# Performance work log

Measured on AMD Instinct MI355X. Metric: run time of the kernel, lower is better.

## Reference

```python
import jax, jax.numpy as jnp
import numpy as np

N_NODES = 100000
N_EDGES = 1600000


def gcn_conv(x, edge_index, W, b, num_nodes):
    # PyG GCNConv: add self-loops, symmetric deg^-1/2 normalization, linear, scatter-add, bias
    h = x @ W  # [N, out]
    loop = jnp.arange(num_nodes)
    row = jnp.concatenate([edge_index[0], loop])
    col = jnp.concatenate([edge_index[1], loop])
    deg = jax.ops.segment_sum(jnp.ones_like(col, dtype=h.dtype), col, num_segments=num_nodes)
    dinv = jnp.where(deg > 0, deg ** -0.5, 0.0)
    norm = dinv[row] * dinv[col]  # [E+N]
    msg = h[row] * norm[:, None]  # gather + scale
    out = jax.ops.segment_sum(msg, col, num_segments=num_nodes)
    return out + b


def setup_inputs() -> dict:
    key = jax.random.key(0)
    ks = jax.random.split(key, 12)
    x = jax.random.normal(ks[0], (N_NODES, 2), dtype=jnp.float32)
    edge_index = jax.random.randint(ks[1], (2, N_EDGES), 0, N_NODES, dtype=jnp.int64)
    edge_attr = jax.random.uniform(ks[2], (N_EDGES, 1), dtype=jnp.float32)
    W1 = jax.random.normal(ks[3], (2, 64), dtype=jnp.float32) * 0.5
    b1 = jnp.zeros((64,), dtype=jnp.float32)
    W2 = jax.random.normal(ks[4], (64, 32), dtype=jnp.float32) * (64 ** -0.5)
    b2 = jnp.zeros((32,), dtype=jnp.float32)
    mW1 = jax.random.normal(ks[5], (65, 16), dtype=jnp.float32) * (65 ** -0.5)
    mb1 = jnp.zeros((16,), dtype=jnp.float32)
    mW2 = jax.random.normal(ks[6], (16, 1), dtype=jnp.float32) * (16 ** -0.5)
    mb2 = jnp.zeros((1,), dtype=jnp.float32)
    return {"x": x, "edge_index": edge_index, "edge_attr": edge_attr,
            "num_nodes": N_NODES,
            "W1": W1, "b1": b1, "W2": W2, "b2": b2,
            "mW1": mW1, "mb1": mb1, "mW2": mW2, "mb2": mb2}


def reference(x, edge_index, edge_attr, num_nodes, W1, b1, W2, b2, mW1, mb1, mW2, mb2):
    h = jax.nn.relu(gcn_conv(x, edge_index, W1, b1, num_nodes))
    h = jax.nn.relu(gcn_conv(h, edge_index, W2, b2, num_nodes))
    row, col = edge_index[0], edge_index[1]
    ef = jnp.concatenate([h[row], h[col], edge_attr], axis=1)  # [E, 65]
    hid = jax.nn.relu(ef @ mW1 + mb1)
    return jax.nn.sigmoid(hid @ mW2 + mb2)  # [E, 1]
```

## Files before the change

kernel.cpp:

```cpp
#include <hip/hip_runtime.h>
#include <hip/hip_fp16.h>
#include <math.h>


__global__ void k_count(const int* __restrict__ col, int* __restrict__ deg, int E) {
    int stride = gridDim.x * blockDim.x;
    for (int e = blockIdx.x * blockDim.x + threadIdx.x; e < E; e += stride)
        atomicAdd(deg + col[e], 1);
}

__global__ void k_scan1(const int* __restrict__ deg, int* __restrict__ start,
                        int* __restrict__ bsum, int N) {
    __shared__ int sd[256];
    int t = threadIdx.x;
    int n = blockIdx.x * 256 + t;
    int d = (n < N) ? deg[n] : 0;
    sd[t] = d;
    __syncthreads();
    for (int off = 1; off < 256; off <<= 1) {
        int tv = (t >= off) ? sd[t - off] : 0;
        __syncthreads();
        sd[t] += tv;
        __syncthreads();
    }
    if (n < N) start[n] = sd[t] - d;
    if (t == 255) bsum[blockIdx.x] = sd[255];
}

__global__ void k_scan2(int* __restrict__ bsum, int nb) {
    __shared__ int sd[512];
    int t = threadIdx.x;
    int d = (t < nb) ? bsum[t] : 0;
    sd[t] = d;
    __syncthreads();
    for (int off = 1; off < 512; off <<= 1) {
        int tv = (t >= off) ? sd[t - off] : 0;
        __syncthreads();
        sd[t] += tv;
        __syncthreads();
    }
    if (t < nb) bsum[t] = sd[t] - d;
}

__global__ void k_scan3(int* __restrict__ start, const int* __restrict__ bsum,
                        int* __restrict__ cursor, const int* __restrict__ deg,
                        const float* __restrict__ x, float* __restrict__ dinv,
                        float* __restrict__ xs, int N) {
    int n = blockIdx.x * 256 + threadIdx.x;
    if (n >= N) return;
    int s = start[n] + bsum[blockIdx.x];
    start[n] = s;
    cursor[n] = s;
    float di = rsqrtf((float)deg[n] + 1.0f);
    dinv[n] = di;
    xs[2 * n] = x[2 * n] * di;
    xs[2 * n + 1] = x[2 * n + 1] * di;
}

__global__ void k_fill(const int* __restrict__ row, const int* __restrict__ col,
                       int* __restrict__ cursor, int* __restrict__ srcidx,
                       int E, int wshift, int nph) {
    int g      = blockIdx.x & 7;
    int tid0   = (blockIdx.x >> 3) * blockDim.x + threadIdx.x;
    int stride = (gridDim.x >> 3) * blockDim.x;
    for (int ph = g; ph < nph; ph += 8) {
        for (int e = tid0; e < E; e += stride) {
            int c = col[e];
            if ((c >> wshift) == ph) {
                int p = atomicAdd(cursor + c, 1);
                srcidx[p] = row[e];
            }
        }
    }
}

__global__ void k_l1l2(const int* __restrict__ start, const int* __restrict__ deg,
                       const int* __restrict__ srcidx,
                       const float* __restrict__ xs, const float* __restrict__ dinv,
                       const float* __restrict__ W1, const float* __restrict__ b1,
                       const float* __restrict__ W2,
                       __half* __restrict__ hs2h, int N) {
    __shared__ float sW1[128], sb1[64], sW2[2048];
    for (int i = threadIdx.x; i < 128;  i += blockDim.x) sW1[i] = W1[i];
    for (int i = threadIdx.x; i < 64;   i += blockDim.x) sb1[i] = b1[i];
    for (int i = threadIdx.x; i < 2048; i += blockDim.x) sW2[i] = W2[i];
    __syncthreads();
    int n = blockIdx.x * 256 + threadIdx.x;
    if (n >= N) return;
    int s = start[n], cnt = deg[n];
    float a0 = xs[2 * n], a1 = xs[2 * n + 1];
    for (int k = 0; k < cnt; ++k) {
        int r = srcidx[s + k];
        a0 += xs[2 * r];
        a1 += xs[2 * r + 1];
    }
    float di = dinv[n];
    a0 *= di; a1 *= di;
    float acc[32];
#pragma unroll
    for (int j = 0; j < 32; ++j) acc[j] = 0.0f;
    for (int k = 0; k < 64; ++k) {
        float h = fmaxf(fmaf(a0, sW1[k], fmaf(a1, sW1[64 + k], sb1[k])), 0.0f);
#pragma unroll
        for (int j = 0; j < 32; ++j) acc[j] = fmaf(h, sW2[k * 32 + j], acc[j]);
    }
    __half2 hb[16];
#pragma unroll
    for (int j = 0; j < 16; ++j)
        hb[j] = __floats2half2_rn(acc[2 * j] * di, acc[2 * j + 1] * di);
    float4* op = (float4*)(hs2h + (size_t)n * 32);
    const float4* ip = (const float4*)hb;
#pragma unroll
    for (int q = 0; q < 4; ++q) op[q] = ip[q];
}

__global__ void k_agg2uv(const int* __restrict__ start, const int* __restrict__ deg,
                         const int* __restrict__ srcidx,
                         const __half* __restrict__ hs2h, const float* __restrict__ dinv,
                         const float* __restrict__ b2, const float* __restrict__ mW1,
                         __half* __restrict__ u16, __half* __restrict__ v16, int N) {
    __shared__ float sA[512], sB[512], sb2[32];
    for (int i = threadIdx.x; i < 512; i += 256) { sA[i] = mW1[i]; sB[i] = mW1[512 + i]; }
    if (threadIdx.x < 32) sb2[threadIdx.x] = b2[threadIdx.x];
    __syncthreads();
    int L  = threadIdx.x & 63;
    int w  = threadIdx.x >> 6;
    int ch = L & 31;
    int h  = L >> 5;
    int n  = blockIdx.x * 4 + w;
    if (n >= N) return;

    int s = start[n], cnt = deg[n];
    float acc0 = (h == 0) ? __half2float(hs2h[(size_t)n * 32 + ch]) : 0.0f;
    float acc1 = 0.0f;
    int k = 0;
    for (; k + 3 < cnt; k += 4) {
        int ra = srcidx[s + k + h];
        int rb = srcidx[s + k + 2 + h];
        acc0 += __half2float(hs2h[(size_t)ra * 32 + ch]);
        acc1 += __half2float(hs2h[(size_t)rb * 32 + ch]);
    }
    for (; k + 1 < cnt; k += 2) {
        int r = srcidx[s + k + h];
        acc0 += __half2float(hs2h[(size_t)r * 32 + ch]);
    }
    if (k < cnt && h == 0) {
        int r = srcidx[s + k];
        acc0 += __half2float(hs2h[(size_t)r * 32 + ch]);
    }
    float acc = acc0 + acc1;
    acc += __shfl_xor(acc, 32);
    float h2 = fmaxf(fmaf(acc, dinv[n], sb2[ch]), 0.0f);

    int jh = L >> 5;
    int os = (L >> 4) & 1;
    int i  = L & 15;
    const float* M = os ? sB : sA;
    float part = 0.0f;
#pragma unroll
    for (int t = 0; t < 16; ++t) {
        int j = jh * 16 + t;
        float hj = __shfl(h2, j);
        part = fmaf(hj, M[j * 16 + i], part);
    }
    part += __shfl_xor(part, 32);
    if (L < 32) {
        __half val = __float2half_rn(part);
        if (os == 0) u16[(size_t)n * 16 + i] = val;
        else         v16[(size_t)n * 16 + i] = val;
    }
}

__device__ inline void unpack8(const float4 f, float* o) {
    const __half2* h2 = (const __half2*)&f;
#pragma unroll
    for (int i = 0; i < 4; ++i) {
        float2 t = __half22float2(h2[i]);
        o[2 * i] = t.x; o[2 * i + 1] = t.y;
    }
}

__global__ void k_edge(const int* __restrict__ row, const int* __restrict__ col,
                       const float* __restrict__ ea,
                       const __half* __restrict__ u16, const __half* __restrict__ v16,
                       const float* __restrict__ mW1, const float* __restrict__ mb1,
                       const float* __restrict__ mW2, const float* __restrict__ mb2,
                       float* __restrict__ out, int E) {
    __shared__ float sC[16], sb1[16], sW2v[16], sb2s;
    if (threadIdx.x < 16) {
        sC[threadIdx.x]   = mW1[64 * 16 + threadIdx.x];
        sb1[threadIdx.x]  = mb1[threadIdx.x];
        sW2v[threadIdx.x] = mW2[threadIdx.x];
    }
    if (threadIdx.x == 0) sb2s = mb2[0];
    __syncthreads();
    int tid    = blockIdx.x * blockDim.x + threadIdx.x;
    int stride = gridDim.x * blockDim.x;
    for (int e0 = tid * 2; e0 < E; e0 += stride * 2) {
        int e1 = e0 + 1;
        bool two = (e1 < E);
        int2 r2 = *(const int2*)(row + e0);
        int2 c2 = *(const int2*)(col + e0);
        float2 a2 = *(const float2*)(ea + e0);
        const float4* up0 = (const float4*)(u16 + (size_t)r2.x * 16);
        const float4* vp0 = (const float4*)(v16 + (size_t)c2.x * 16);
        const float4* up1 = (const float4*)(u16 + (size_t)r2.y * 16);
        const float4* vp1 = (const float4*)(v16 + (size_t)c2.y * 16);
        float4 ua0 = up0[0], ub0 = up0[1];
        float4 va0 = vp0[0], vb0 = vp0[1];
        float4 ua1 = up1[0], ub1 = up1[1];
        float4 va1 = vp1[0], vb1 = vp1[1];
        float uf0[16], vf0[16], uf1[16], vf1[16];
        unpack8(ua0, uf0); unpack8(ub0, uf0 + 8);
        unpack8(va0, vf0); unpack8(vb0, vf0 + 8);
        unpack8(ua1, uf1); unpack8(ub1, uf1 + 8);
        unpack8(va1, vf1); unpack8(vb1, vf1 + 8);
        float s0 = sb2s, s1 = sb2s;
#pragma unroll
        for (int i = 0; i < 16; ++i) {
            float t0 = fmaf(a2.x, sC[i], sb1[i]);
            float t1 = fmaf(a2.y, sC[i], sb1[i]);
            float h0 = fmaxf(uf0[i] + vf0[i] + t0, 0.0f);
            float h1 = fmaxf(uf1[i] + vf1[i] + t1, 0.0f);
            s0 = fmaf(h0, sW2v[i], s0);
            s1 = fmaf(h1, sW2v[i], s1);
        }
        float o0 = 1.0f / (1.0f + expf(-s0));
        float o1 = 1.0f / (1.0f + expf(-s1));
        if (two) {
            *(float2*)(out + e0) = make_float2(o0, o1);
        } else {
            out[e0] = o0;
        }
    }
}

extern "C" void kernel_launch(void* const* d_in, const int* in_sizes, int n_in,
                              void* d_out, int out_size, void* d_ws, size_t ws_size,
                              hipStream_t stream) {
    const float* x   = (const float*)d_in[0];
    const int*   ei  = (const int*)d_in[1];
    const float* ea  = (const float*)d_in[2];
    const float* W1  = (const float*)d_in[4];
    const float* b1  = (const float*)d_in[5];
    const float* W2  = (const float*)d_in[6];
    const float* b2  = (const float*)d_in[7];
    const float* mW1 = (const float*)d_in[8];
    const float* mb1 = (const float*)d_in[9];
    const float* mW2 = (const float*)d_in[10];
    const float* mb2 = (const float*)d_in[11];
    float* out = (float*)d_out;

    int N = in_sizes[0] / 2;
    int E = in_sizes[2];
    const int* row = ei;
    const int* col = ei + E;

    int clog = 0; while ((1u << clog) < (unsigned)N) ++clog;
    int wshift = clog > 3 ? clog - 3 : 0;
    int nph = ((N - 1) >> wshift) + 1;

    int* deg    = (int*)d_ws;
    int* start  = deg + N;
    int* cursor = start + N;
    int* bsum   = cursor + N;
    int* srcidx = bsum + 1024;
    float* dinv = (float*)(srcidx + E);
    float* xs   = dinv + (size_t)N;
    __half* hs2h = (__half*)(xs + (size_t)2 * N);
    __half* u16  = hs2h + (size_t)32 * N;
    __half* v16  = u16 + (size_t)16 * N;

    int nb_n = (N + 255) / 256;

    hipMemsetAsync(deg, 0, (size_t)N * sizeof(int), stream);
    k_count<<<2048, 256, 0, stream>>>(col, deg, E);
    k_scan1<<<nb_n, 256, 0, stream>>>(deg, start, bsum, N);
    k_scan2<<<1, 512, 0, stream>>>(bsum, nb_n);
    k_scan3<<<nb_n, 256, 0, stream>>>(start, bsum, cursor, deg, x, dinv, xs, N);
    k_fill <<<2048, 256, 0, stream>>>(row, col, cursor, srcidx, E, wshift, nph);
    k_l1l2 <<<nb_n, 256, 0, stream>>>(start, deg, srcidx, xs, dinv, W1, b1, W2, hs2h, N);
    k_agg2uv<<<(N + 3) / 4, 256, 0, stream>>>(start, deg, srcidx, hs2h, dinv, b2, mW1, u16, v16, N);
    k_edge <<<2048, 256, 0, stream>>>(row, col, ea, u16, v16, mW1, mb1, mW2, mb2, out, E);
}
```

Baseline: 365.8 us.

## Split edge MLP into two half-width passes for cache-resident node tables

The per-node u/v projection tables are split into two 8-channel halves, and the edge kernel runs twice. The first pass writes partial logits to a per-edge scratch buffer, and the second adds the rest and applies the sigmoid. Each pass's gather table is half as large, so the randomly gathered node data fits better in cache. The cost is re-reading the edge indices and edge attributes, plus an extra write and read of per-edge partial sums. The aggregation loop is also unrolled to four independent accumulators to expose more memory-level parallelism.

```diff
diff --git a/kernel.cpp b/kernel.cpp
--- a/kernel.cpp
+++ b/kernel.cpp
@@ -118,7 +118,8 @@
                          const int* __restrict__ srcidx,
                          const __half* __restrict__ hs2h, const float* __restrict__ dinv,
                          const float* __restrict__ b2, const float* __restrict__ mW1,
-                         __half* __restrict__ u16, __half* __restrict__ v16, int N) {
+                         __half* __restrict__ uA, __half* __restrict__ uB,
+                         __half* __restrict__ vA, __half* __restrict__ vB, int N) {
     __shared__ float sA[512], sB[512], sb2[32];
     for (int i = threadIdx.x; i < 512; i += 256) { sA[i] = mW1[i]; sB[i] = mW1[512 + i]; }
     if (threadIdx.x < 32) sb2[threadIdx.x] = b2[threadIdx.x];
@@ -132,13 +133,17 @@
 
     int s = start[n], cnt = deg[n];
     float acc0 = (h == 0) ? __half2float(hs2h[(size_t)n * 32 + ch]) : 0.0f;
-    float acc1 = 0.0f;
+    float acc1 = 0.0f, acc2 = 0.0f, acc3 = 0.0f;
     int k = 0;
-    for (; k + 3 < cnt; k += 4) {
+    for (; k + 7 < cnt; k += 8) {
         int ra = srcidx[s + k + h];
         int rb = srcidx[s + k + 2 + h];
+        int rc = srcidx[s + k + 4 + h];
+        int rd = srcidx[s + k + 6 + h];
         acc0 += __half2float(hs2h[(size_t)ra * 32 + ch]);
         acc1 += __half2float(hs2h[(size_t)rb * 32 + ch]);
+        acc2 += __half2float(hs2h[(size_t)rc * 32 + ch]);
+        acc3 += __half2float(hs2h[(size_t)rd * 32 + ch]);
     }
     for (; k + 1 < cnt; k += 2) {
         int r = srcidx[s + k + h];
@@ -148,7 +153,7 @@
         int r = srcidx[s + k];
         acc0 += __half2float(hs2h[(size_t)r * 32 + ch]);
     }
-    float acc = acc0 + acc1;
+    float acc = (acc0 + acc1) + (acc2 + acc3);
     acc += __shfl_xor(acc, 32);
     float h2 = fmaxf(fmaf(acc, dinv[n], sb2[ch]), 0.0f);
 
@@ -166,71 +171,82 @@
     part += __shfl_xor(part, 32);
     if (L < 32) {
         __half val = __float2half_rn(part);
-        if (os == 0) u16[(size_t)n * 16 + i] = val;
-        else         v16[(size_t)n * 16 + i] = val;
-    }
-}
-
-__device__ inline void unpack8(const float4 f, float* o) {
+        int ii = i & 7;
+        __half* base = os ? ((i < 8) ? vA : vB) : ((i < 8) ? uA : uB);
+        base[(size_t)n * 8 + ii] = val;
+    }
+}
+
+__device__ inline void unpack4(const float2 f, float* o) {
     const __half2* h2 = (const __half2*)&f;
 #pragma unroll
-    for (int i = 0; i < 4; ++i) {
+    for (int i = 0; i < 2; ++i) {
         float2 t = __half22float2(h2[i]);
         o[2 * i] = t.x; o[2 * i + 1] = t.y;
     }
 }
 
-__global__ void k_edge(const int* __restrict__ row, const int* __restrict__ col,
-                       const float* __restrict__ ea,
-                       const __half* __restrict__ u16, const __half* __restrict__ v16,
-                       const float* __restrict__ mW1, const float* __restrict__ mb1,
-                       const float* __restrict__ mW2, const float* __restrict__ mb2,
-                       float* __restrict__ out, int E) {
-    __shared__ float sC[16], sb1[16], sW2v[16], sb2s;
-    if (threadIdx.x < 16) {
-        sC[threadIdx.x]   = mW1[64 * 16 + threadIdx.x];
-        sb1[threadIdx.x]  = mb1[threadIdx.x];
-        sW2v[threadIdx.x] = mW2[threadIdx.x];
+template <int PASS>
+__global__ void k_edge_half(const int* __restrict__ row, const int* __restrict__ col,
+                            const float* __restrict__ ea,
+                            const __half* __restrict__ ut, const __half* __restrict__ vt,
+                            const float* __restrict__ mW1, const float* __restrict__ mb1,
+                            const float* __restrict__ mW2,  const float* __restrict__ mb2,
+                            float* __restrict__ spart, float* __restrict__ out, int E) {
+    __shared__ float sC[8], sb1[8], sW2v[8], sb2s;
+    if (threadIdx.x < 8) {
+        int i = threadIdx.x + PASS * 8;
+        sC[threadIdx.x]   = mW1[64 * 16 + i];
+        sb1[threadIdx.x]  = mb1[i];
+        sW2v[threadIdx.x] = mW2[i];
     }
     if (threadIdx.x == 0) sb2s = mb2[0];
     __syncthreads();
     int tid    = blockIdx.x * blockDim.x + threadIdx.x;
     int stride = gridDim.x * blockDim.x;
     for (int e0 = tid * 2; e0 < E; e0 += stride * 2) {
-        int e1 = e0 + 1;
-        bool two = (e1 < E);
+        bool two = (e0 + 1 < E);
         int2 r2 = *(const int2*)(row + e0);
         int2 c2 = *(const int2*)(col + e0);
         float2 a2 = *(const float2*)(ea + e0);
-        const float4* up0 = (const float4*)(u16 + (size_t)r2.x * 16);
-        const float4* vp0 = (const float4*)(v16 + (size_t)c2.x * 16);
-        const float4* up1 = (const float4*)(u16 + (size_t)r2.y * 16);
-        const float4* vp1 = (const float4*)(v16 + (size_t)c2.y * 16);
-        float4 ua0 = up0[0], ub0 = up0[1];
-        float4 va0 = vp0[0], vb0 = vp0[1];
-        float4 ua1 = up1[0], ub1 = up1[1];
-        float4 va1 = vp1[0], vb1 = vp1[1];
-        float uf0[16], vf0[16], uf1[16], vf1[16];
-        unpack8(ua0, uf0); unpack8(ub0, uf0 + 8);
-        unpack8(va0, vf0); unpack8(vb0, vf0 + 8);
-        unpack8(ua1, uf1); unpack8(ub1, uf1 + 8);
-        unpack8(va1, vf1); unpack8(vb1, vf1 + 8);
-        float s0 = sb2s, s1 = sb2s;
-#pragma unroll
-        for (int i = 0; i < 16; ++i) {
+        float2 u0 = *(const float2*)(ut + (size_t)r2.x * 8);
+        float2 v0 = *(const float2*)(vt + (size_t)c2.x * 8);
+        float2 u1 = *(const float2*)(ut + (size_t)r2.y * 8);
+        float2 v1 = *(const float2*)(vt + (size_t)c2.y * 8);
+        float uf0[4], vf0[4], uf1[4], vf1[4];
+        unpack4(u0, uf0); unpack4(v0, vf0);
+        unpack4(u1, uf1); unpack4(v1, vf1);
+        float2 u0b = *(const float2*)(ut + (size_t)r2.x * 8 + 4);
+        float2 v0b = *(const float2*)(vt + (size_t)c2.x * 8 + 4);
+        float2 u1b = *(const float2*)(ut + (size_t)r2.y * 8 + 4);
+        float2 v1b = *(const float2*)(vt + (size_t)c2.y * 8 + 4);
+        float uf0b[4], vf0b[4], uf1b[4], vf1b[4];
+        unpack4(u0b, uf0b); unpack4(v0b, vf0b);
+        unpack4(u1b, uf1b); unpack4(v1b, vf1b);
+        float s0 = (PASS == 0) ? sb2s : spart[e0];
+        float s1 = (PASS == 0) ? sb2s : (two ? spart[e0 + 1] : 0.0f);
+#pragma unroll
+        for (int i = 0; i < 4; ++i) {
             float t0 = fmaf(a2.x, sC[i], sb1[i]);
             float t1 = fmaf(a2.y, sC[i], sb1[i]);
-            float h0 = fmaxf(uf0[i] + vf0[i] + t0, 0.0f);
-            float h1 = fmaxf(uf1[i] + vf1[i] + t1, 0.0f);
-            s0 = fmaf(h0, sW2v[i], s0);
-            s1 = fmaf(h1, sW2v[i], s1);
+            s0 = fmaf(fmaxf(uf0[i] + vf0[i] + t0, 0.0f), sW2v[i], s0);
+            s1 = fmaf(fmaxf(uf1[i] + vf1[i] + t1, 0.0f), sW2v[i], s1);
         }
-        float o0 = 1.0f / (1.0f + expf(-s0));
-        float o1 = 1.0f / (1.0f + expf(-s1));
-        if (two) {
-            *(float2*)(out + e0) = make_float2(o0, o1);
+#pragma unroll
+        for (int i = 0; i < 4; ++i) {
+            float t0 = fmaf(a2.x, sC[i + 4], sb1[i + 4]);
+            float t1 = fmaf(a2.y, sC[i + 4], sb1[i + 4]);
+            s0 = fmaf(fmaxf(uf0b[i] + vf0b[i] + t0, 0.0f), sW2v[i + 4], s0);
+            s1 = fmaf(fmaxf(uf1b[i] + vf1b[i] + t1, 0.0f), sW2v[i + 4], s1);
+        }
+        if (PASS == 0) {
+            if (two) *(float2*)(spart + e0) = make_float2(s0, s1);
+            else     spart[e0] = s0;
         } else {
-            out[e0] = o0;
+            float o0 = 1.0f / (1.0f + expf(-s0));
+            float o1 = 1.0f / (1.0f + expf(-s1));
+            if (two) *(float2*)(out + e0) = make_float2(o0, o1);
+            else     out[e0] = o0;
         }
     }
 }
@@ -267,9 +283,12 @@
     int* srcidx = bsum + 1024;
     float* dinv = (float*)(srcidx + E);
     float* xs   = dinv + (size_t)N;
-    __half* hs2h = (__half*)(xs + (size_t)2 * N);
-    __half* u16  = hs2h + (size_t)32 * N;
-    __half* v16  = u16 + (size_t)16 * N;
+    float* spart = xs + (size_t)2 * N;
+    __half* hs2h = (__half*)(spart + (size_t)E);
+    __half* uA   = hs2h + (size_t)32 * N;
+    __half* uB   = uA + (size_t)8 * N;
+    __half* vA   = uB + (size_t)8 * N;
+    __half* vB   = vA + (size_t)8 * N;
 
     int nb_n = (N + 255) / 256;
 
@@ -280,6 +299,10 @@
     k_scan3<<<nb_n, 256, 0, stream>>>(start, bsum, cursor, deg, x, dinv, xs, N);
     k_fill <<<2048, 256, 0, stream>>>(row, col, cursor, srcidx, E, wshift, nph);
     k_l1l2 <<<nb_n, 256, 0, stream>>>(start, deg, srcidx, xs, dinv, W1, b1, W2, hs2h, N);
-    k_agg2uv<<<(N + 3) / 4, 256, 0, stream>>>(start, deg, srcidx, hs2h, dinv, b2, mW1, u16, v16, N);
-    k_edge <<<2048, 256, 0, stream>>>(row, col, ea, u16, v16, mW1, mb1, mW2, mb2, out, E);
-}
+    k_agg2uv<<<(N + 3) / 4, 256, 0, stream>>>(start, deg, srcidx, hs2h, dinv, b2, mW1,
+                                              uA, uB, vA, vB, N);
+    k_edge_half<0><<<2048, 256, 0, stream>>>(row, col, ea, uA, vA, mW1, mb1, mW2, mb2,
+                                             spart, out, E);
+    k_edge_half<1><<<2048, 256, 0, stream>>>(row, col, ea, uB, vB, mW1, mb1, mW2, mb2,
+                                             spart, out, E);
+}
```

New measurement: 364.2 us. No clear change (-0.4%).
